# Performance work log

Hardware: AMD Instinct MI355X
Metric: run time of the kernel (lower is better)

Reference implementation:

```python
import jax, jax.numpy as jnp
import numpy as np

N_HEAD = 16
EPS = 1e-5

def _layernorm(x, g, b):
    m = jnp.mean(x, axis=-1, keepdims=True)
    v = jnp.mean((x - m) ** 2, axis=-1, keepdims=True)
    return (x - m) * jax.lax.rsqrt(v + EPS) * g + b

def _gru_gate(h, X, w, u, bz):
    # w, u: [3, C, C] stacked (r, z, h) matrices; matches torch.tensordot(X, W, dims=1)
    r = jax.nn.sigmoid(X @ w[0] + h @ u[0])
    z = jax.nn.sigmoid(X @ w[1] + h @ u[1] - bz)
    h_next = jnp.tanh(X @ w[2] + (h * r) @ u[2])
    return (1.0 - z) * h + z * h_next

def setup_inputs() -> dict:
    key = jax.random.key(0)
    B, T, C = 4, 1024, 1024
    ks = jax.random.split(key, 32)
    s = 0.02
    inp = {
        'q': jax.random.normal(ks[0], (B, T, C), jnp.float32),
        'k': jax.random.normal(ks[1], (B, T, C), jnp.float32),
        'v': jax.random.normal(ks[2], (B, T, C), jnp.float32),
        'ln1_g': jnp.ones((C,), jnp.float32), 'ln1_b': jnp.zeros((C,), jnp.float32),
        'ln2_g': jnp.ones((C,), jnp.float32), 'ln2_b': jnp.zeros((C,), jnp.float32),
        'Wq': jax.random.normal(ks[3], (C, C), jnp.float32) * s, 'bq': jnp.zeros((C,), jnp.float32),
        'Wk': jax.random.normal(ks[4], (C, C), jnp.float32) * s, 'bk': jnp.zeros((C,), jnp.float32),
        'Wv': jax.random.normal(ks[5], (C, C), jnp.float32) * s, 'bv': jnp.zeros((C,), jnp.float32),
        'Wp': jax.random.normal(ks[6], (C, C), jnp.float32) * s, 'bp': jnp.zeros((C,), jnp.float32),
        'W1': jax.random.normal(ks[7], (C, 2 * C), jnp.float32) * s, 'b1': jnp.zeros((2 * C,), jnp.float32),
        'W2': jax.random.normal(ks[8], (2 * C, C), jnp.float32) * s, 'b2': jnp.zeros((C,), jnp.float32),
        'g1_w': jax.random.normal(ks[9], (3, C, C), jnp.float32) * s,
        'g1_u': jax.random.normal(ks[10], (3, C, C), jnp.float32) * s,
        'g1_bz': jnp.full((C,), 2.0, jnp.float32),  # init_gru_gate_bias
        'g2_w': jax.random.normal(ks[11], (3, C, C), jnp.float32) * s,
        'g2_u': jax.random.normal(ks[12], (3, C, C), jnp.float32) * s,
        'g2_bz': jnp.full((C,), 2.0, jnp.float32),
    }
    return inp

def reference(q, k, v, ln1_g, ln1_b, ln2_g, ln2_b, Wq, bq, Wk, bk, Wv, bv, Wp, bp,
              W1, b1, W2, b2, g1_w, g1_u, g1_bz, g2_w, g2_u, g2_bz):
    B, T, C = q.shape
    D = C // N_HEAD
    qn = _layernorm(q, ln1_g, ln1_b)
    kn = _layernorm(k, ln1_g, ln1_b)
    vn = _layernorm(v, ln1_g, ln1_b)
    qh = (qn @ Wq + bq).reshape(B, T, N_HEAD, D)
    kh = (kn @ Wk + bk).reshape(B, T, N_HEAD, D)
    vh = (vn @ Wv + bv).reshape(B, T, N_HEAD, D)
    att = jnp.einsum('bqhd,bkhd->bhqk', qh, kh) * (1.0 / np.sqrt(D))
    causal = jnp.tril(jnp.ones((T, T), bool))  # mask[-Tq:, :Tk]
    att_scores = jnp.where(causal, att, -jnp.inf)
    att_probs = jax.nn.softmax(att_scores, axis=-1)
    y = jnp.einsum('bhqk,bkhd->bqhd', att_probs, vh).reshape(B, T, C)
    att_out = y @ Wp + bp
    x = _gru_gate(q, att_out, g1_w, g1_u, g1_bz)
    h = _layernorm(x, ln2_g, ln2_b)
    mlp = jax.nn.gelu(h @ W1 + b1, approximate=False) @ W2 + b2
    x = _gru_gate(x, mlp, g2_w, g2_u, g2_bz)
    return (x, att_scores)
```

## Files before the change

### kernel.cpp

```cpp
#include <hip/hip_runtime.h>
#include <math.h>

#define TDIM 1024
#define CDIM 1024
#define NHEAD 16
#define HD 64
#define MROWS 4096

#define MASK_NEG -1.0e30f

typedef __attribute__((ext_vector_type(8))) __bf16 bf16x8;
typedef __attribute__((ext_vector_type(4))) float f32x4;

__device__ __forceinline__ float sigf(float x) { return 1.0f / (1.0f + expf(-x)); }
__device__ __forceinline__ float geluf(float x) { return x * 0.5f * (1.0f + erff(x * 0.7071067811865475f)); }
__device__ __forceinline__ float bf2f(unsigned short u) {
    union { unsigned u; float f; } x; x.u = ((unsigned)u) << 16; return x.f;
}
__device__ __forceinline__ unsigned short f2bf(float f) {
    union { float f; unsigned u; } x; x.f = f;
    unsigned r = x.u + 0x7FFFu + ((x.u >> 16) & 1u);
    return (unsigned short)(r >> 16);
}

__global__ __launch_bounds__(256) void wconv_t(const float* __restrict__ in,
                                               unsigned short* __restrict__ out,
                                               int K, int N) {
    const float* inb = in + (size_t)blockIdx.z * K * N;
    unsigned short* outb = out + (size_t)blockIdx.z * K * N;
    __shared__ float tile[32][33];
    int t = threadIdx.x;
    int r = t >> 3, c = (t & 7) * 4;
    int kb = blockIdx.y * 32, nb = blockIdx.x * 32;
    float4 vv = *(const float4*)(inb + (size_t)(kb + r) * N + nb + c);
    tile[r][c + 0] = vv.x; tile[r][c + 1] = vv.y; tile[r][c + 2] = vv.z; tile[r][c + 3] = vv.w;
    __syncthreads();
    ushort4 o;
    o.x = f2bf(tile[c + 0][r]); o.y = f2bf(tile[c + 1][r]);
    o.z = f2bf(tile[c + 2][r]); o.w = f2bf(tile[c + 3][r]);
    *(ushort4*)(outb + (size_t)(nb + r) * K + kb + c) = o;
}

__global__ __launch_bounds__(256) void f2bf_kernel(const float* __restrict__ in,
                                                   unsigned short* __restrict__ out) {
    size_t i = ((size_t)blockIdx.x * 256 + threadIdx.x) * 4;
    float4 v = *(const float4*)(in + i);
    ushort4 o; o.x = f2bf(v.x); o.y = f2bf(v.y); o.z = f2bf(v.z); o.w = f2bf(v.w);
    *(ushort4*)(out + i) = o;
}

template <int INBF16>
__global__ __launch_bounds__(256) void ln_kernel(const void* __restrict__ xin,
                                                 const float* __restrict__ g,
                                                 const float* __restrict__ b,
                                                 unsigned short* __restrict__ out) {
    int row = blockIdx.x;
    int t = threadIdx.x;
    float4 v;
    if (INBF16) {
        const unsigned short* xr = (const unsigned short*)xin + (size_t)row * CDIM;
        ushort4 u = *(const ushort4*)(xr + t * 4);
        v.x = bf2f(u.x); v.y = bf2f(u.y); v.z = bf2f(u.z); v.w = bf2f(u.w);
    } else {
        const float* xr = (const float*)xin + (size_t)row * CDIM;
        v = *(const float4*)(xr + t * 4);
    }
    __shared__ float red[256];
    red[t] = v.x + v.y + v.z + v.w;
    __syncthreads();
    for (int o = 128; o > 0; o >>= 1) { if (t < o) red[t] += red[t + o]; __syncthreads(); }
    float mean = red[0] * (1.0f / CDIM);
    __syncthreads();
    float dx = v.x - mean, dy = v.y - mean, dz = v.z - mean, dw = v.w - mean;
    red[t] = dx * dx + dy * dy + dz * dz + dw * dw;
    __syncthreads();
    for (int o = 128; o > 0; o >>= 1) { if (t < o) red[t] += red[t + o]; __syncthreads(); }
    float var = red[0] * (1.0f / CDIM);
    float inv = 1.0f / sqrtf(var + 1e-5f);
    float4 gv = *(const float4*)(g + t * 4);
    float4 bv = *(const float4*)(b + t * 4);
    ushort4 o4;
    o4.x = f2bf(dx * inv * gv.x + bv.x);
    o4.y = f2bf(dy * inv * gv.y + bv.y);
    o4.z = f2bf(dz * inv * gv.z + bv.z);
    o4.w = f2bf(dw * inv * gv.w + bv.w);
    *(ushort4*)(out + (size_t)row * CDIM + t * 4) = o4;
}

template <int GELU>
__global__ __launch_bounds__(256) void mfma_gemm(const unsigned short* __restrict__ A,
                                                 const unsigned short* __restrict__ Bt,
                                                 const float* __restrict__ bias,
                                                 unsigned short* __restrict__ C,
                                                 int M, int N, int K, int outmode) {
    __shared__ unsigned short As[2][128 * 32];
    __shared__ unsigned short Bs[2][128 * 32];
    int t = threadIdx.x;
    int wave = t >> 6, lane = t & 63;
    int nwg = gridDim.x * gridDim.y;
    int hID = blockIdx.y * gridDim.x + blockIdx.x;
    int nl = (hID & 7) * (nwg >> 3) + (hID >> 3);
    int bx = nl % gridDim.x, by = nl / gridDim.x;
    int m0 = by * 128, n0 = bx * 128;
    int wx = wave & 1, wy = wave >> 1;
    int srow = lane >> 2;
    int scol = (lane & 3) * 8;
    int fr = lane & 15;
    int fq = (lane >> 4) * 8;

    f32x4 acc[4][4] = {};

#define STAGE_AB(buf, k0v)                                                                         \
    {                                                                                              \
        _Pragma("unroll")                                                                          \
        for (int i = 0; i < 2; i++) {                                                              \
            int rt = (wave * 2 + i) * 16 + srow;                                                   \
            __builtin_amdgcn_global_load_lds(                                                      \
                (const __attribute__((address_space(1))) void*)(A + (size_t)(m0 + rt) * K + (k0v) + scol), \
                (__attribute__((address_space(3))) void*)(As[buf] + rt * 32 + scol), 16, 0, 0);    \
            __builtin_amdgcn_global_load_lds(                                                      \
                (const __attribute__((address_space(1))) void*)(Bt + (size_t)(n0 + rt) * K + (k0v) + scol), \
                (__attribute__((address_space(3))) void*)(Bs[buf] + rt * 32 + scol), 16, 0, 0);    \
        }                                                                                          \
    }

    STAGE_AB(0, 0);
    int cur = 0;
    for (int k0 = 0; k0 < K; k0 += 32) {
        __syncthreads();
        if (k0 + 32 < K) STAGE_AB(cur ^ 1, k0 + 32);

        bf16x8 af[4], bfr[4];
#pragma unroll
        for (int mi = 0; mi < 4; mi++)
            af[mi] = *(const bf16x8*)(As[cur] + (wy * 64 + mi * 16 + fr) * 32 + fq);
#pragma unroll
        for (int ni = 0; ni < 4; ni++)
            bfr[ni] = *(const bf16x8*)(Bs[cur] + (wx * 64 + ni * 16 + fr) * 32 + fq);
#pragma unroll
        for (int mi = 0; mi < 4; mi++)
#pragma unroll
            for (int ni = 0; ni < 4; ni++)
                acc[mi][ni] = __builtin_amdgcn_mfma_f32_16x16x32_bf16(af[mi], bfr[ni], acc[mi][ni], 0, 0, 0);
        cur ^= 1;
    }
#undef STAGE_AB

    int col_l = lane & 15, quad = lane >> 4;
#pragma unroll
    for (int ni = 0; ni < 4; ni++) {
        int c = n0 + wx * 64 + ni * 16 + col_l;
        float bb = bias ? bias[c] : 0.0f;
#pragma unroll
        for (int mi = 0; mi < 4; mi++) {
#pragma unroll
            for (int r = 0; r < 4; r++) {
                int row = m0 + wy * 64 + mi * 16 + quad * 4 + r;
                float vv = acc[mi][ni][r] + bb;
                if (GELU) vv = geluf(vv);
                size_t idx;
                if (outmode == 1) {
                    int bI = row >> 10, tt2 = row & 1023, hh = c >> 6, d = c & 63;
                    idx = (((size_t)(bI * NHEAD + hh)) * TDIM + tt2) * HD + d;
                } else if (outmode == 2) {
                    int bI = row >> 10, tt2 = row & 1023, hh = c >> 6, d = c & 63;
                    idx = (((size_t)(bI * NHEAD + hh)) * HD + d) * TDIM + tt2;
                } else {
                    idx = (size_t)row * N + c;
                }
                C[idx] = f2bf(vv);
            }
        }
    }
}

__global__ __launch_bounds__(256, 4) void attn_fused(const unsigned short* __restrict__ Q,
                                                     const unsigned short* __restrict__ K,
                                                     const unsigned short* __restrict__ Vt,
                                                     float* __restrict__ S,
                                                     unsigned short* __restrict__ Y) {
    int hID = blockIdx.y * gridDim.x + blockIdx.x;
    int nlw = (hID & 7) * 128 + (hID >> 3);
    int qt = nlw & 15, bh = nlw >> 4;
    int q0 = qt * 64;
    int t = threadIdx.x, w = t >> 6, lane = t & 63;
    int l15 = lane & 15, quad = lane >> 4;
    int l7 = lane & 7, l3 = lane >> 3;

    __shared__ unsigned short Ks[2][4096];
    __shared__ unsigned short Vs[2][4096];
    __shared__ unsigned short PsU[4096];

    const unsigned short* Qb = Q + ((size_t)bh * TDIM + q0) * HD;
    const unsigned short* Kb0 = K + (size_t)bh * TDIM * HD;
    const unsigned short* Vtb = Vt + (size_t)bh * HD * TDIM;
    float* Sb = S + (size_t)bh * TDIM * TDIM;

    int dstoff = w * 512 + lane * 8;

    bf16x8 aq[2];
    {
        int qrow = w * 16 + l15;
#pragma unroll
        for (int kk = 0; kk < 2; kk++)
            aq[kk] = *(const bf16x8*)(Qb + (size_t)qrow * HD + kk * 32 + quad * 8);
    }

    float m_run[4], l_run[4];
    f32x4 yacc[4];
#pragma unroll
    for (int r = 0; r < 4; r++) { m_run[r] = MASK_NEG; l_run[r] = 0.f; }
#pragma unroll
    for (int nd = 0; nd < 4; nd++) yacc[nd] = (f32x4){0.f, 0.f, 0.f, 0.f};

    unsigned short* Psw = PsU + w * 1024;

#define STAGE_KV(buf, ktile)                                                                        \
    {                                                                                               \
        _Pragma("unroll")                                                                           \
        for (int it = 0; it < 2; it++) {                                                            \
            int row = it * 32 + w * 8 + l3;                                        \
            __builtin_amdgcn_global_load_lds(                                                       \
                (const __attribute__((address_space(1))) void*)(Kb0 + (size_t)((ktile) * 64 + row) * HD + ((l7 ^ l3) << 3)), \
                (__attribute__((address_space(3))) void*)(Ks[buf] + it * 2048 + dstoff), 16, 0, 0); \
            __builtin_amdgcn_global_load_lds(                                                       \
                (const __attribute__((address_space(1))) void*)(Vtb + (size_t)row * TDIM + (ktile) * 64 + ((l7 ^ l3) << 3)), \
                (__attribute__((address_space(3))) void*)(Vs[buf] + it * 2048 + dstoff), 16, 0, 0); \
        }                                                                                           \
    }

    STAGE_KV(0, 0);
    int cur = 0;

    for (int kt = 0; kt <= qt; kt++) {
        __syncthreads();
        if (kt < qt) STAGE_KV(cur ^ 1, kt + 1);

        f32x4 sA[4];
#pragma unroll
        for (int n = 0; n < 4; n++) sA[n] = (f32x4){0.f, 0.f, 0.f, 0.f};
#pragma unroll
        for (int kk = 0; kk < 2; kk++) {
#pragma unroll
            for (int n = 0; n < 4; n++) {
                int krow = n * 16 + l15;
                bf16x8 bk = *(const bf16x8*)(Ks[cur] + krow * 64 + ((((kk * 64 + quad * 16)) ^ ((krow & 7) << 4)) >> 1));
                sA[n] = __builtin_amdgcn_mfma_f32_16x16x32_bf16(aq[kk], bk, sA[n], 0, 0, 0);
            }
        }

        int kbase = kt * 64;
        bool diag = (kt == qt);
#pragma unroll
        for (int n = 0; n < 4; n++) {
            int kg = kbase + n * 16 + l15;
#pragma unroll
            for (int r = 0; r < 4; r++) {
                int qg = q0 + w * 16 + quad * 4 + r;
                float x = sA[n][r] * 0.125f;
                if (diag && kg > qg) x = MASK_NEG;
                sA[n][r] = x;
                Sb[(size_t)qg * TDIM + kg] = x;
            }
        }

#pragma unroll
        for (int r = 0; r < 4; r++) {
            float m = fmaxf(fmaxf(sA[0][r], sA[1][r]), fmaxf(sA[2][r], sA[3][r]));
            m = fmaxf(m, __shfl_xor(m, 1));
            m = fmaxf(m, __shfl_xor(m, 2));
            m = fmaxf(m, __shfl_xor(m, 4));
            m = fmaxf(m, __shfl_xor(m, 8));
            float mn = fmaxf(m_run[r], m);
            float sc = expf(m_run[r] - mn);
            m_run[r] = mn;
            float ls = 0.f;
#pragma unroll
            for (int n = 0; n < 4; n++) {
                float p = expf(sA[n][r] - mn);
                sA[n][r] = p;
                ls += p;
            }
            ls += __shfl_xor(ls, 1);
            ls += __shfl_xor(ls, 2);
            ls += __shfl_xor(ls, 4);
            ls += __shfl_xor(ls, 8);
            l_run[r] = l_run[r] * sc + ls;
#pragma unroll
            for (int nd = 0; nd < 4; nd++) yacc[nd][r] *= sc;
        }

#pragma unroll
        for (int n = 0; n < 4; n++) {
            int kk2 = n * 16 + l15;
#pragma unroll
            for (int r = 0; r < 4; r++) {
                int qq = quad * 4 + r;
                Psw[qq * 64 + (((kk2 * 2) ^ ((qq & 7) << 4)) >> 1)] = f2bf(sA[n][r]);
            }
        }

#pragma unroll
        for (int kk = 0; kk < 2; kk++) {
            bf16x8 pa = *(const bf16x8*)(Psw + l15 * 64 + ((((kk * 64 + quad * 16)) ^ ((l15 & 7) << 4)) >> 1));
#pragma unroll
            for (int nd = 0; nd < 4; nd++) {
                int dr = nd * 16 + l15;
                bf16x8 bv = *(const bf16x8*)(Vs[cur] + dr * 64 + ((((kk * 64 + quad * 16)) ^ ((dr & 7) << 4)) >> 1));
                yacc[nd] = __builtin_amdgcn_mfma_f32_16x16x32_bf16(pa, bv, yacc[nd], 0, 0, 0);
            }
        }
        cur ^= 1;
    }
#undef STAGE_KV

    int bI = bh >> 4, h = bh & 15;
#pragma unroll
    for (int r = 0; r < 4; r++) {
        float inv = 1.0f / l_run[r];
        int row = bI * TDIM + q0 + w * 16 + quad * 4 + r;
#pragma unroll
        for (int nd = 0; nd < 4; nd++)
            Y[(size_t)row * CDIM + h * HD + nd * 16 + l15] = f2bf(yacc[nd][r] * inv);
    }

    int kfill = (qt + 1) * 64;
    if (kfill < TDIM) {
        float4 m4 = make_float4(MASK_NEG, MASK_NEG, MASK_NEG, MASK_NEG);
        int rr = t >> 4, cc = (t & 15) * 4;
#pragma unroll
        for (int rp = 0; rp < 4; rp++) {
            float* Srow = Sb + (size_t)(q0 + rp * 16 + rr) * TDIM;
            for (int k4 = kfill + cc; k4 < TDIM; k4 += 64)
                *(float4*)(Srow + k4) = m4;
        }
    }
}

__global__ __launch_bounds__(256) void ew_r(const unsigned short* __restrict__ A, int ldA,
                                            const unsigned short* __restrict__ B,
                                            const unsigned short* __restrict__ h,
                                            unsigned short* __restrict__ out) {
    int row = blockIdx.x, c = threadIdx.x * 4;
    size_t ia = (size_t)row * ldA + c;
    size_t i = (size_t)row * CDIM + c;
    ushort4 a = *(const ushort4*)(A + ia);
    ushort4 b = *(const ushort4*)(B + i);
    ushort4 hh = *(const ushort4*)(h + i);
    ushort4 o;
    o.x = f2bf(bf2f(hh.x) * sigf(bf2f(a.x) + bf2f(b.x)));
    o.y = f2bf(bf2f(hh.y) * sigf(bf2f(a.y) + bf2f(b.y)));
    o.z = f2bf(bf2f(hh.z) * sigf(bf2f(a.z) + bf2f(b.z)));
    o.w = f2bf(bf2f(hh.w) * sigf(bf2f(a.w) + bf2f(b.w)));
    *(ushort4*)(out + i) = o;
}

__global__ __launch_bounds__(256) void ew_tanh(const unsigned short* __restrict__ A, int ldA,
                                               const unsigned short* __restrict__ B,
                                               unsigned short* __restrict__ out) {
    int row = blockIdx.x, c = threadIdx.x * 4;
    size_t ia = (size_t)row * ldA + c;
    size_t i = (size_t)row * CDIM + c;
    ushort4 a = *(const ushort4*)(A + ia);
    ushort4 b = *(const ushort4*)(B + i);
    ushort4 o;
    o.x = f2bf(tanhf(bf2f(a.x) + bf2f(b.x)));
    o.y = f2bf(tanhf(bf2f(a.y) + bf2f(b.y)));
    o.z = f2bf(tanhf(bf2f(a.z) + bf2f(b.z)));
    o.w = f2bf(tanhf(bf2f(a.w) + bf2f(b.w)));
    *(ushort4*)(out + i) = o;
}

template <int F32OUT>
__global__ __launch_bounds__(256) void ew_final(const unsigned short* __restrict__ A, int ldA,
                                                const unsigned short* __restrict__ B,
                                                const unsigned short* __restrict__ T,
                                                const unsigned short* __restrict__ h,
                                                const float* __restrict__ bz,
                                                void* __restrict__ out) {
    int row = blockIdx.x, c = threadIdx.x * 4;
    size_t ia = (size_t)row * ldA + c;
    size_t i = (size_t)row * CDIM + c;
    ushort4 a = *(const ushort4*)(A + ia);
    ushort4 b = *(const ushort4*)(B + i);
    ushort4 tv = *(const ushort4*)(T + i);
    ushort4 hh = *(const ushort4*)(h + i);
    float4 bzv = *(const float4*)(bz + c);
    float z, o0, o1, o2, o3;
    z = sigf(bf2f(a.x) + bf2f(b.x) - bzv.x); o0 = (1.f - z) * bf2f(hh.x) + z * bf2f(tv.x);
    z = sigf(bf2f(a.y) + bf2f(b.y) - bzv.y); o1 = (1.f - z) * bf2f(hh.y) + z * bf2f(tv.y);
    z = sigf(bf2f(a.z) + bf2f(b.z) - bzv.z); o2 = (1.f - z) * bf2f(hh.z) + z * bf2f(tv.z);
    z = sigf(bf2f(a.w) + bf2f(b.w) - bzv.w); o3 = (1.f - z) * bf2f(hh.w) + z * bf2f(tv.w);
    if (F32OUT) {
        float4 o = make_float4(o0, o1, o2, o3);
        *(float4*)((float*)out + i) = o;
    } else {
        ushort4 o; o.x = f2bf(o0); o.y = f2bf(o1); o.z = f2bf(o2); o.w = f2bf(o3);
        *(ushort4*)((unsigned short*)out + i) = o;
    }
}

extern "C" void kernel_launch(void* const* d_in, const int* in_sizes, int n_in,
                              void* d_out, int out_size, void* d_ws, size_t ws_size,
                              hipStream_t stream) {
    const float* q    = (const float*)d_in[0];
    const float* k    = (const float*)d_in[1];
    const float* v    = (const float*)d_in[2];
    const float* ln1g = (const float*)d_in[3];
    const float* ln1b = (const float*)d_in[4];
    const float* ln2g = (const float*)d_in[5];
    const float* ln2b = (const float*)d_in[6];
    const float* Wq   = (const float*)d_in[7];
    const float* bq   = (const float*)d_in[8];
    const float* Wk   = (const float*)d_in[9];
    const float* bk   = (const float*)d_in[10];
    const float* Wv   = (const float*)d_in[11];
    const float* bv   = (const float*)d_in[12];
    const float* Wp   = (const float*)d_in[13];
    const float* bp   = (const float*)d_in[14];
    const float* W1   = (const float*)d_in[15];
    const float* b1   = (const float*)d_in[16];
    const float* W2   = (const float*)d_in[17];
    const float* b2   = (const float*)d_in[18];
    const float* g1w  = (const float*)d_in[19];
    const float* g1u  = (const float*)d_in[20];
    const float* g1bz = (const float*)d_in[21];
    const float* g2w  = (const float*)d_in[22];
    const float* g2u  = (const float*)d_in[23];
    const float* g2bz = (const float*)d_in[24];

    float* out_x = (float*)d_out;
    float* out_s = out_x + (size_t)MROWS * CDIM;

    unsigned short* w = (unsigned short*)d_ws;
    const size_t MM = (size_t)CDIM * CDIM;
    unsigned short* wWq  = w;
    unsigned short* wWk  = w + 1 * MM;
    unsigned short* wWv  = w + 2 * MM;
    unsigned short* wWp  = w + 3 * MM;
    unsigned short* wW1  = w + 4 * MM;
    unsigned short* wW2  = w + 6 * MM;
    unsigned short* wg1w = w + 8 * MM;
    unsigned short* wg1u = w + 11 * MM;
    unsigned short* wg2w = w + 14 * MM;
    unsigned short* wg2u = w + 17 * MM;
    unsigned short* act = w + 20 * MM;
    const size_t SLOT = (size_t)MROWS * CDIM;
    unsigned short* a0 = act + 0 * SLOT;
    unsigned short* a1 = act + 1 * SLOT;
    unsigned short* a2 = act + 2 * SLOT;
    unsigned short* a3 = act + 3 * SLOT;
    unsigned short* a4 = act + 4 * SLOT;
    unsigned short* a5 = act + 5 * SLOT;

    dim3 blk(256);
    dim3 g_c(32, 32, 1), g_c3(32, 32, 3);
    dim3 g_gemm(CDIM / 128, MROWS / 128);
    dim3 g_gemm_w1(2 * CDIM / 128, MROWS / 128);
    dim3 g_gemm_g(3 * CDIM / 128, MROWS / 128);
    dim3 g_attn(TDIM / 64, 4 * NHEAD);
    dim3 g_ew(MROWS);

    wconv_t<<<g_c, blk, 0, stream>>>(Wq, wWq, 1024, 1024);
    wconv_t<<<g_c, blk, 0, stream>>>(Wk, wWk, 1024, 1024);
    wconv_t<<<g_c, blk, 0, stream>>>(Wv, wWv, 1024, 1024);
    wconv_t<<<g_c, blk, 0, stream>>>(Wp, wWp, 1024, 1024);
    wconv_t<<<dim3(64, 32, 1), blk, 0, stream>>>(W1, wW1, 1024, 2048);
    wconv_t<<<dim3(32, 64, 1), blk, 0, stream>>>(W2, wW2, 2048, 1024);
    wconv_t<<<g_c3, blk, 0, stream>>>(g1w, wg1w, 1024, 1024);
    wconv_t<<<g_c3, blk, 0, stream>>>(g1u, wg1u, 1024, 1024);
    wconv_t<<<g_c3, blk, 0, stream>>>(g2w, wg2w, 1024, 1024);
    wconv_t<<<g_c3, blk, 0, stream>>>(g2u, wg2u, 1024, 1024);
    f2bf_kernel<<<g_ew, blk, 0, stream>>>(q, a5);

    ln_kernel<0><<<MROWS, blk, 0, stream>>>(q, ln1g, ln1b, a0);
    mfma_gemm<0><<<g_gemm, blk, 0, stream>>>(a0, wWq, bq, a1, MROWS, CDIM, CDIM, 1);
    ln_kernel<0><<<MROWS, blk, 0, stream>>>(k, ln1g, ln1b, a0);
    mfma_gemm<0><<<g_gemm, blk, 0, stream>>>(a0, wWk, bk, a2, MROWS, CDIM, CDIM, 1);
    ln_kernel<0><<<MROWS, blk, 0, stream>>>(v, ln1g, ln1b, a0);
    mfma_gemm<0><<<g_gemm, blk, 0, stream>>>(a0, wWv, bv, a3, MROWS, CDIM, CDIM, 2);

    attn_fused<<<g_attn, blk, 0, stream>>>(a1, a2, a3, out_s, a0);

    mfma_gemm<0><<<g_gemm, blk, 0, stream>>>(a0, wWp, bp, a1, MROWS, CDIM, CDIM, 0);

    mfma_gemm<0><<<g_gemm_g, blk, 0, stream>>>(a1, wg1w, nullptr, a2, MROWS, 3 * CDIM, CDIM, 0);
    mfma_gemm<0><<<g_gemm, blk, 0, stream>>>(a5, wg1u + 0 * MM, nullptr, a0, MROWS, CDIM, CDIM, 0);
    ew_r<<<g_ew, blk, 0, stream>>>(a2, 3 * CDIM, a0, a5, a0);
    mfma_gemm<0><<<g_gemm, blk, 0, stream>>>(a0, wg1u + 2 * MM, nullptr, a1, MROWS, CDIM, CDIM, 0);
    ew_tanh<<<g_ew, blk, 0, stream>>>(a2 + 2 * CDIM, 3 * CDIM, a1, a1);
    mfma_gemm<0><<<g_gemm, blk, 0, stream>>>(a5, wg1u + 1 * MM, nullptr, a0, MROWS, CDIM, CDIM, 0);
    ew_final<0><<<g_ew, blk, 0, stream>>>(a2 + CDIM, 3 * CDIM, a0, a1, a5, g1bz, a0);

    ln_kernel<1><<<MROWS, blk, 0, stream>>>(a0, ln2g, ln2b, a1);
    mfma_gemm<1><<<g_gemm_w1, blk, 0, stream>>>(a1, wW1, b1, a2, MROWS, 2 * CDIM, CDIM, 0);
    mfma_gemm<0><<<g_gemm, blk, 0, stream>>>(a2, wW2, b2, a1, MROWS, CDIM, 2 * CDIM, 0);

    mfma_gemm<0><<<g_gemm_g, blk, 0, stream>>>(a1, wg2w, nullptr, a2, MROWS, 3 * CDIM, CDIM, 0);
    mfma_gemm<0><<<g_gemm, blk, 0, stream>>>(a0, wg2u + 0 * MM, nullptr, a5, MROWS, CDIM, CDIM, 0);
    ew_r<<<g_ew, blk, 0, stream>>>(a2, 3 * CDIM, a5, a0, a5);
    mfma_gemm<0><<<g_gemm, blk, 0, stream>>>(a5, wg2u + 2 * MM, nullptr, a1, MROWS, CDIM, CDIM, 0);
    ew_tanh<<<g_ew, blk, 0, stream>>>(a2 + 2 * CDIM, 3 * CDIM, a1, a1);
    mfma_gemm<0><<<g_gemm, blk, 0, stream>>>(a0, wg2u + 1 * MM, nullptr, a5, MROWS, CDIM, CDIM, 0);
    ew_final<1><<<g_ew, blk, 0, stream>>>(a2 + CDIM, 3 * CDIM, a5, a1, a0, g2bz, out_x);
}
```

Measured before the change: 1.049 ms.

## Batch QKV and GRU gate GEMMs, fuse elementwise tails and LayerNorm, cut launches

The three input LayerNorms now run in one launch, and the Q/K/V projections run as a single z-batched GEMM whose output layout is chosen per slice. The GRU u_r and u_z GEMMs merge into one 2C-wide GEMM, and tanh is folded into the final gate kernel, which also computes the second LayerNorm. Weight conversions are grouped into fewer launches, and s_setprio hints are added around the attention MFMA sections. The aim is fewer kernel launches and fewer activation round trips through memory, at the cost of more buffers and more complex indexing.

```diff
diff --git a/kernel.cpp b/kernel.cpp
--- a/kernel.cpp
+++ b/kernel.cpp
@@ -23,11 +23,18 @@
     return (unsigned short)(r >> 16);
 }
 
-__global__ __launch_bounds__(256) void wconv_t(const float* __restrict__ in,
+__global__ __launch_bounds__(256) void wconv_t(const float* __restrict__ i0,
+                                               const float* __restrict__ i1,
+                                               const float* __restrict__ i2,
+                                               const float* __restrict__ i3,
+                                               int gper,
                                                unsigned short* __restrict__ out,
                                                int K, int N) {
-    const float* inb = in + (size_t)blockIdx.z * K * N;
-    unsigned short* outb = out + (size_t)blockIdx.z * K * N;
+    int z = blockIdx.z;
+    int sel = z / gper, sub = z % gper;
+    const float* ps = sel == 0 ? i0 : sel == 1 ? i1 : sel == 2 ? i2 : i3;
+    const float* inb = ps + (size_t)sub * K * N;
+    unsigned short* outb = out + (size_t)z * K * N;
     __shared__ float tile[32][33];
     int t = threadIdx.x;
     int r = t >> 3, c = (t & 7) * 4;
@@ -49,22 +56,16 @@
     *(ushort4*)(out + i) = o;
 }
 
-template <int INBF16>
-__global__ __launch_bounds__(256) void ln_kernel(const void* __restrict__ xin,
-                                                 const float* __restrict__ g,
-                                                 const float* __restrict__ b,
-                                                 unsigned short* __restrict__ out) {
-    int row = blockIdx.x;
+__global__ __launch_bounds__(256) void ln3_kernel(const float* __restrict__ p0,
+                                                  const float* __restrict__ p1,
+                                                  const float* __restrict__ p2,
+                                                  const float* __restrict__ g,
+                                                  const float* __restrict__ b,
+                                                  unsigned short* __restrict__ out) {
+    int row = blockIdx.x, z = blockIdx.y;
+    const float* xr = (z == 0 ? p0 : z == 1 ? p1 : p2) + (size_t)row * CDIM;
     int t = threadIdx.x;
-    float4 v;
-    if (INBF16) {
-        const unsigned short* xr = (const unsigned short*)xin + (size_t)row * CDIM;
-        ushort4 u = *(const ushort4*)(xr + t * 4);
-        v.x = bf2f(u.x); v.y = bf2f(u.y); v.z = bf2f(u.z); v.w = bf2f(u.w);
-    } else {
-        const float* xr = (const float*)xin + (size_t)row * CDIM;
-        v = *(const float4*)(xr + t * 4);
-    }
+    float4 v = *(const float4*)(xr + t * 4);
     __shared__ float red[256];
     red[t] = v.x + v.y + v.z + v.w;
     __syncthreads();
@@ -84,17 +85,26 @@
     o4.y = f2bf(dy * inv * gv.y + bv.y);
     o4.z = f2bf(dz * inv * gv.z + bv.z);
     o4.w = f2bf(dw * inv * gv.w + bv.w);
-    *(ushort4*)(out + (size_t)row * CDIM + t * 4) = o4;
+    *(ushort4*)(out + ((size_t)z * MROWS + row) * CDIM + t * 4) = o4;
 }
 
 template <int GELU>
-__global__ __launch_bounds__(256) void mfma_gemm(const unsigned short* __restrict__ A,
-                                                 const unsigned short* __restrict__ Bt,
-                                                 const float* __restrict__ bias,
-                                                 unsigned short* __restrict__ C,
+__global__ __launch_bounds__(256) void mfma_gemm(const unsigned short* __restrict__ A0, size_t aStride,
+                                                 const unsigned short* __restrict__ Bt0, size_t bStride,
+                                                 const float* __restrict__ b0,
+                                                 const float* __restrict__ b1,
+                                                 const float* __restrict__ b2,
+                                                 unsigned short* __restrict__ C0, size_t cStride,
                                                  int M, int N, int K, int outmode) {
     __shared__ unsigned short As[2][128 * 32];
     __shared__ unsigned short Bs[2][128 * 32];
+    int z = blockIdx.z;
+    const unsigned short* A = A0 + (size_t)z * aStride;
+    const unsigned short* Bt = Bt0 + (size_t)z * bStride;
+    unsigned short* C = C0 + (size_t)z * cStride;
+    const float* bias = z == 0 ? b0 : z == 1 ? b1 : b2;
+    int om = (outmode == 3) ? (z == 2 ? 2 : 1) : outmode;
+
     int t = threadIdx.x;
     int wave = t >> 6, lane = t & 63;
     int nwg = gridDim.x * gridDim.y;
@@ -159,10 +169,10 @@
                 float vv = acc[mi][ni][r] + bb;
                 if (GELU) vv = geluf(vv);
                 size_t idx;
-                if (outmode == 1) {
+                if (om == 1) {
                     int bI = row >> 10, tt2 = row & 1023, hh = c >> 6, d = c & 63;
                     idx = (((size_t)(bI * NHEAD + hh)) * TDIM + tt2) * HD + d;
-                } else if (outmode == 2) {
+                } else if (om == 2) {
                     int bI = row >> 10, tt2 = row & 1023, hh = c >> 6, d = c & 63;
                     idx = (((size_t)(bI * NHEAD + hh)) * HD + d) * TDIM + tt2;
                 } else {
@@ -239,6 +249,7 @@
         f32x4 sA[4];
 #pragma unroll
         for (int n = 0; n < 4; n++) sA[n] = (f32x4){0.f, 0.f, 0.f, 0.f};
+        __builtin_amdgcn_s_setprio(1);
 #pragma unroll
         for (int kk = 0; kk < 2; kk++) {
 #pragma unroll
@@ -248,6 +259,7 @@
                 sA[n] = __builtin_amdgcn_mfma_f32_16x16x32_bf16(aq[kk], bk, sA[n], 0, 0, 0);
             }
         }
+        __builtin_amdgcn_s_setprio(0);
 
         int kbase = kt * 64;
         bool diag = (kt == qt);
@@ -300,6 +312,7 @@
             }
         }
 
+        __builtin_amdgcn_s_setprio(1);
 #pragma unroll
         for (int kk = 0; kk < 2; kk++) {
             bf16x8 pa = *(const bf16x8*)(Psw + l15 * 64 + ((((kk * 64 + quad * 16)) ^ ((l15 & 7) << 4)) >> 1));
@@ -310,6 +323,7 @@
                 yacc[nd] = __builtin_amdgcn_mfma_f32_16x16x32_bf16(pa, bv, yacc[nd], 0, 0, 0);
             }
         }
+        __builtin_amdgcn_s_setprio(0);
         cur ^= 1;
     }
 #undef STAGE_KV
@@ -338,14 +352,13 @@
 }
 
 __global__ __launch_bounds__(256) void ew_r(const unsigned short* __restrict__ A, int ldA,
-                                            const unsigned short* __restrict__ B,
+                                            const unsigned short* __restrict__ B, int ldB,
                                             const unsigned short* __restrict__ h,
                                             unsigned short* __restrict__ out) {
     int row = blockIdx.x, c = threadIdx.x * 4;
-    size_t ia = (size_t)row * ldA + c;
+    ushort4 a = *(const ushort4*)(A + (size_t)row * ldA + c);
+    ushort4 b = *(const ushort4*)(B + (size_t)row * ldB + c);
     size_t i = (size_t)row * CDIM + c;
-    ushort4 a = *(const ushort4*)(A + ia);
-    ushort4 b = *(const ushort4*)(B + i);
     ushort4 hh = *(const ushort4*)(h + i);
     ushort4 o;
     o.x = f2bf(bf2f(hh.x) * sigf(bf2f(a.x) + bf2f(b.x)));
@@ -355,48 +368,57 @@
     *(ushort4*)(out + i) = o;
 }
 
-__global__ __launch_bounds__(256) void ew_tanh(const unsigned short* __restrict__ A, int ldA,
-                                               const unsigned short* __restrict__ B,
-                                               unsigned short* __restrict__ out) {
-    int row = blockIdx.x, c = threadIdx.x * 4;
-    size_t ia = (size_t)row * ldA + c;
+template <int F32OUT, int DOLN>
+__global__ __launch_bounds__(256) void ew_final2(const unsigned short* __restrict__ A, int ldA,
+                                                 const unsigned short* __restrict__ B, int ldB,
+                                                 const unsigned short* __restrict__ B3v,
+                                                 const unsigned short* __restrict__ h,
+                                                 const float* __restrict__ bz,
+                                                 void* __restrict__ out,
+                                                 const float* __restrict__ lng,
+                                                 const float* __restrict__ lnb,
+                                                 unsigned short* __restrict__ lnout) {
+    int row = blockIdx.x, t = threadIdx.x, c = t * 4;
+    size_t ia = (size_t)row * ldA, ib = (size_t)row * ldB;
     size_t i = (size_t)row * CDIM + c;
-    ushort4 a = *(const ushort4*)(A + ia);
-    ushort4 b = *(const ushort4*)(B + i);
-    ushort4 o;
-    o.x = f2bf(tanhf(bf2f(a.x) + bf2f(b.x)));
-    o.y = f2bf(tanhf(bf2f(a.y) + bf2f(b.y)));
-    o.z = f2bf(tanhf(bf2f(a.z) + bf2f(b.z)));
-    o.w = f2bf(tanhf(bf2f(a.w) + bf2f(b.w)));
-    *(ushort4*)(out + i) = o;
-}
-
-template <int F32OUT>
-__global__ __launch_bounds__(256) void ew_final(const unsigned short* __restrict__ A, int ldA,
-                                                const unsigned short* __restrict__ B,
-                                                const unsigned short* __restrict__ T,
-                                                const unsigned short* __restrict__ h,
-                                                const float* __restrict__ bz,
-                                                void* __restrict__ out) {
-    int row = blockIdx.x, c = threadIdx.x * 4;
-    size_t ia = (size_t)row * ldA + c;
-    size_t i = (size_t)row * CDIM + c;
-    ushort4 a = *(const ushort4*)(A + ia);
-    ushort4 b = *(const ushort4*)(B + i);
-    ushort4 tv = *(const ushort4*)(T + i);
+    ushort4 a2 = *(const ushort4*)(A + ia + 1024 + c);
+    ushort4 b2 = *(const ushort4*)(B + ib + 1024 + c);
+    ushort4 a3 = *(const ushort4*)(A + ia + 2048 + c);
+    ushort4 b3 = *(const ushort4*)(B3v + i);
     ushort4 hh = *(const ushort4*)(h + i);
     float4 bzv = *(const float4*)(bz + c);
-    float z, o0, o1, o2, o3;
-    z = sigf(bf2f(a.x) + bf2f(b.x) - bzv.x); o0 = (1.f - z) * bf2f(hh.x) + z * bf2f(tv.x);
-    z = sigf(bf2f(a.y) + bf2f(b.y) - bzv.y); o1 = (1.f - z) * bf2f(hh.y) + z * bf2f(tv.y);
-    z = sigf(bf2f(a.z) + bf2f(b.z) - bzv.z); o2 = (1.f - z) * bf2f(hh.z) + z * bf2f(tv.z);
-    z = sigf(bf2f(a.w) + bf2f(b.w) - bzv.w); o3 = (1.f - z) * bf2f(hh.w) + z * bf2f(tv.w);
+    float zz, o0, o1, o2, o3;
+    zz = sigf(bf2f(a2.x) + bf2f(b2.x) - bzv.x); o0 = (1.f - zz) * bf2f(hh.x) + zz * tanhf(bf2f(a3.x) + bf2f(b3.x));
+    zz = sigf(bf2f(a2.y) + bf2f(b2.y) - bzv.y); o1 = (1.f - zz) * bf2f(hh.y) + zz * tanhf(bf2f(a3.y) + bf2f(b3.y));
+    zz = sigf(bf2f(a2.z) + bf2f(b2.z) - bzv.z); o2 = (1.f - zz) * bf2f(hh.z) + zz * tanhf(bf2f(a3.z) + bf2f(b3.z));
+    zz = sigf(bf2f(a2.w) + bf2f(b2.w) - bzv.w); o3 = (1.f - zz) * bf2f(hh.w) + zz * tanhf(bf2f(a3.w) + bf2f(b3.w));
     if (F32OUT) {
-        float4 o = make_float4(o0, o1, o2, o3);
-        *(float4*)((float*)out + i) = o;
+        *(float4*)((float*)out + i) = make_float4(o0, o1, o2, o3);
     } else {
         ushort4 o; o.x = f2bf(o0); o.y = f2bf(o1); o.z = f2bf(o2); o.w = f2bf(o3);
         *(ushort4*)((unsigned short*)out + i) = o;
+    }
+    if (DOLN) {
+        __shared__ float red[256];
+        red[t] = o0 + o1 + o2 + o3;
+        __syncthreads();
+        for (int o = 128; o > 0; o >>= 1) { if (t < o) red[t] += red[t + o]; __syncthreads(); }
+        float mean = red[0] * (1.0f / CDIM);
+        __syncthreads();
+        float dx = o0 - mean, dy = o1 - mean, dz = o2 - mean, dw = o3 - mean;
+        red[t] = dx * dx + dy * dy + dz * dz + dw * dw;
+        __syncthreads();
+        for (int o = 128; o > 0; o >>= 1) { if (t < o) red[t] += red[t + o]; __syncthreads(); }
+        float var = red[0] * (1.0f / CDIM);
+        float inv = 1.0f / sqrtf(var + 1e-5f);
+        float4 gv = *(const float4*)(lng + c);
+        float4 bv = *(const float4*)(lnb + c);
+        ushort4 o4;
+        o4.x = f2bf(dx * inv * gv.x + bv.x);
+        o4.y = f2bf(dy * inv * gv.y + bv.y);
+        o4.z = f2bf(dz * inv * gv.z + bv.z);
+        o4.w = f2bf(dw * inv * gv.w + bv.w);
+        *(ushort4*)(lnout + i) = o4;
     }
 }
 
@@ -435,8 +457,6 @@
     unsigned short* w = (unsigned short*)d_ws;
     const size_t MM = (size_t)CDIM * CDIM;
     unsigned short* wWq  = w;
-    unsigned short* wWk  = w + 1 * MM;
-    unsigned short* wWv  = w + 2 * MM;
     unsigned short* wWp  = w + 3 * MM;
     unsigned short* wW1  = w + 4 * MM;
     unsigned short* wW2  = w + 6 * MM;
@@ -446,61 +466,62 @@
     unsigned short* wg2u = w + 17 * MM;
     unsigned short* act = w + 20 * MM;
     const size_t SLOT = (size_t)MROWS * CDIM;
-    unsigned short* a0 = act + 0 * SLOT;
-    unsigned short* a1 = act + 1 * SLOT;
-    unsigned short* a2 = act + 2 * SLOT;
-    unsigned short* a3 = act + 3 * SLOT;
-    unsigned short* a4 = act + 4 * SLOT;
-    unsigned short* a5 = act + 5 * SLOT;
+    unsigned short* s0 = act + 0 * SLOT;
+    unsigned short* s1 = act + 1 * SLOT;
+    unsigned short* s2 = act + 2 * SLOT;
+    unsigned short* s3 = act + 3 * SLOT;
+    unsigned short* s4 = act + 4 * SLOT;
+    unsigned short* s5 = act + 5 * SLOT;
+    unsigned short* s6 = act + 6 * SLOT;
+    unsigned short* s7 = act + 7 * SLOT;
+    unsigned short* s8 = act + 8 * SLOT;
+    (void)s4;
 
     dim3 blk(256);
-    dim3 g_c(32, 32, 1), g_c3(32, 32, 3);
-    dim3 g_gemm(CDIM / 128, MROWS / 128);
-    dim3 g_gemm_w1(2 * CDIM / 128, MROWS / 128);
-    dim3 g_gemm_g(3 * CDIM / 128, MROWS / 128);
-    dim3 g_attn(TDIM / 64, 4 * NHEAD);
+    dim3 g_gemm(8, 32, 1);
+    dim3 g_gemm3(8, 32, 3);
+    dim3 g_gemm_w1(16, 32, 1);
+    dim3 g_gemm_g(24, 32, 1);
+    dim3 g_attn(16, 64);
     dim3 g_ew(MROWS);
 
-    wconv_t<<<g_c, blk, 0, stream>>>(Wq, wWq, 1024, 1024);
-    wconv_t<<<g_c, blk, 0, stream>>>(Wk, wWk, 1024, 1024);
-    wconv_t<<<g_c, blk, 0, stream>>>(Wv, wWv, 1024, 1024);
-    wconv_t<<<g_c, blk, 0, stream>>>(Wp, wWp, 1024, 1024);
-    wconv_t<<<dim3(64, 32, 1), blk, 0, stream>>>(W1, wW1, 1024, 2048);
-    wconv_t<<<dim3(32, 64, 1), blk, 0, stream>>>(W2, wW2, 2048, 1024);
-    wconv_t<<<g_c3, blk, 0, stream>>>(g1w, wg1w, 1024, 1024);
-    wconv_t<<<g_c3, blk, 0, stream>>>(g1u, wg1u, 1024, 1024);
-    wconv_t<<<g_c3, blk, 0, stream>>>(g2w, wg2w, 1024, 1024);
-    wconv_t<<<g_c3, blk, 0, stream>>>(g2u, wg2u, 1024, 1024);
-    f2bf_kernel<<<g_ew, blk, 0, stream>>>(q, a5);
-
-    ln_kernel<0><<<MROWS, blk, 0, stream>>>(q, ln1g, ln1b, a0);
-    mfma_gemm<0><<<g_gemm, blk, 0, stream>>>(a0, wWq, bq, a1, MROWS, CDIM, CDIM, 1);
-    ln_kernel<0><<<MROWS, blk, 0, stream>>>(k, ln1g, ln1b, a0);
-    mfma_gemm<0><<<g_gemm, blk, 0, stream>>>(a0, wWk, bk, a2, MROWS, CDIM, CDIM, 1);
-    ln_kernel<0><<<MROWS, blk, 0, stream>>>(v, ln1g, ln1b, a0);
-    mfma_gemm<0><<<g_gemm, blk, 0, stream>>>(a0, wWv, bv, a3, MROWS, CDIM, CDIM, 2);
-
-    attn_fused<<<g_attn, blk, 0, stream>>>(a1, a2, a3, out_s, a0);
-
-    mfma_gemm<0><<<g_gemm, blk, 0, stream>>>(a0, wWp, bp, a1, MROWS, CDIM, CDIM, 0);
-
-    mfma_gemm<0><<<g_gemm_g, blk, 0, stream>>>(a1, wg1w, nullptr, a2, MROWS, 3 * CDIM, CDIM, 0);
-    mfma_gemm<0><<<g_gemm, blk, 0, stream>>>(a5, wg1u + 0 * MM, nullptr, a0, MROWS, CDIM, CDIM, 0);
-    ew_r<<<g_ew, blk, 0, stream>>>(a2, 3 * CDIM, a0, a5, a0);
-    mfma_gemm<0><<<g_gemm, blk, 0, stream>>>(a0, wg1u + 2 * MM, nullptr, a1, MROWS, CDIM, CDIM, 0);
-    ew_tanh<<<g_ew, blk, 0, stream>>>(a2 + 2 * CDIM, 3 * CDIM, a1, a1);
-    mfma_gemm<0><<<g_gemm, blk, 0, stream>>>(a5, wg1u + 1 * MM, nullptr, a0, MROWS, CDIM, CDIM, 0);
-    ew_final<0><<<g_ew, blk, 0, stream>>>(a2 + CDIM, 3 * CDIM, a0, a1, a5, g1bz, a0);
-
-    ln_kernel<1><<<MROWS, blk, 0, stream>>>(a0, ln2g, ln2b, a1);
-    mfma_gemm<1><<<g_gemm_w1, blk, 0, stream>>>(a1, wW1, b1, a2, MROWS, 2 * CDIM, CDIM, 0);
-    mfma_gemm<0><<<g_gemm, blk, 0, stream>>>(a2, wW2, b2, a1, MROWS, CDIM, 2 * CDIM, 0);
-
-    mfma_gemm<0><<<g_gemm_g, blk, 0, stream>>>(a1, wg2w, nullptr, a2, MROWS, 3 * CDIM, CDIM, 0);
-    mfma_gemm<0><<<g_gemm, blk, 0, stream>>>(a0, wg2u + 0 * MM, nullptr, a5, MROWS, CDIM, CDIM, 0);
-    ew_r<<<g_ew, blk, 0, stream>>>(a2, 3 * CDIM, a5, a0, a5);
-    mfma_gemm<0><<<g_gemm, blk, 0, stream>>>(a5, wg2u + 2 * MM, nullptr, a1, MROWS, CDIM, CDIM, 0);
-    ew_tanh<<<g_ew, blk, 0, stream>>>(a2 + 2 * CDIM, 3 * CDIM, a1, a1);
-    mfma_gemm<0><<<g_gemm, blk, 0, stream>>>(a0, wg2u + 1 * MM, nullptr, a5, MROWS, CDIM, CDIM, 0);
-    ew_final<1><<<g_ew, blk, 0, stream>>>(a2 + CDIM, 3 * CDIM, a5, a1, a0, g2bz, out_x);
-}
+    wconv_t<<<dim3(32, 32, 4), blk, 0, stream>>>(Wq, Wk, Wv, Wp, 1, wWq, 1024, 1024);
+    wconv_t<<<dim3(32, 32, 12), blk, 0, stream>>>(g1w, g1u, g2w, g2u, 3, wg1w, 1024, 1024);
+    wconv_t<<<dim3(64, 32, 1), blk, 0, stream>>>(W1, W1, W1, W1, 1, wW1, 1024, 2048);
+    wconv_t<<<dim3(32, 64, 1), blk, 0, stream>>>(W2, W2, W2, W2, 1, wW2, 2048, 1024);
+    f2bf_kernel<<<g_ew, blk, 0, stream>>>(q, s6);
+
+    ln3_kernel<<<dim3(MROWS, 3), blk, 0, stream>>>(q, k, v, ln1g, ln1b, s0);
+    mfma_gemm<0><<<g_gemm3, blk, 0, stream>>>(s0, SLOT, wWq, MM, bq, bk, bv, s3, SLOT,
+                                              MROWS, CDIM, CDIM, 3);
+
+    attn_fused<<<g_attn, blk, 0, stream>>>(s3, s4, s5, out_s, s0);
+
+    mfma_gemm<0><<<g_gemm, blk, 0, stream>>>(s0, 0, wWp, 0, bp, bp, bp, s1, 0,
+                                             MROWS, CDIM, CDIM, 0);
+
+    mfma_gemm<0><<<g_gemm_g, blk, 0, stream>>>(s1, 0, wg1w, 0, nullptr, nullptr, nullptr,
+                                               s2, 0, MROWS, 3 * CDIM, CDIM, 0);
+    mfma_gemm<0><<<g_gemm_w1, blk, 0, stream>>>(s6, 0, wg1u, 0, nullptr, nullptr, nullptr,
+                                                s0, 0, MROWS, 2 * CDIM, CDIM, 0);
+    ew_r<<<g_ew, blk, 0, stream>>>(s2, 3 * CDIM, s0, 2 * CDIM, s6, s5);
+    mfma_gemm<0><<<g_gemm, blk, 0, stream>>>(s5, 0, wg1u + 2 * MM, 0, nullptr, nullptr, nullptr,
+                                             s7, 0, MROWS, CDIM, CDIM, 0);
+    ew_final2<0, 1><<<g_ew, blk, 0, stream>>>(s2, 3 * CDIM, s0, 2 * CDIM, s7, s6, g1bz,
+                                              s5, ln2g, ln2b, s8);
+
+    mfma_gemm<1><<<g_gemm_w1, blk, 0, stream>>>(s8, 0, wW1, 0, b1, b1, b1, s0, 0,
+                                                MROWS, 2 * CDIM, CDIM, 0);
+    mfma_gemm<0><<<g_gemm, blk, 0, stream>>>(s0, 0, wW2, 0, b2, b2, b2, s6, 0,
+                                             MROWS, CDIM, 2 * CDIM, 0);
+
+    mfma_gemm<0><<<g_gemm_g, blk, 0, stream>>>(s6, 0, wg2w, 0, nullptr, nullptr, nullptr,
+                                               s0, 0, MROWS, 3 * CDIM, CDIM, 0);
+    mfma_gemm<0><<<g_gemm_w1, blk, 0, stream>>>(s5, 0, wg2u, 0, nullptr, nullptr, nullptr,
+                                                s3, 0, MROWS, 2 * CDIM, CDIM, 0);
+    ew_r<<<g_ew, blk, 0, stream>>>(s0, 3 * CDIM, s3, 2 * CDIM, s5, s7);
+    mfma_gemm<0><<<g_gemm, blk, 0, stream>>>(s7, 0, wg2u + 2 * MM, 0, nullptr, nullptr, nullptr,
+                                             s8, 0, MROWS, CDIM, CDIM, 0);
+    ew_final2<1, 0><<<g_ew, blk, 0, stream>>>(s0, 3 * CDIM, s3, 2 * CDIM, s8, s5, g2bz,
+                                              out_x, nullptr, nullptr, nullptr);
+}
```

After: 909.8 us. -13.2%, faster.
